# Performance work log

Measured on AMD Instinct MI355X. Metric: run time of the kernel, lower is better.

## Reference

```python
import jax, jax.numpy as jnp
import numpy as np

N_HEAD = 16
D_HEAD = 64
N_GROUPS = 4
D_EMBED = 1024
ROPE_N = 32
B, T = 2, 2048


def apply_rope(x, cos, sin):
    # x: (..., T, ROPE_N); cos/sin: (T, ROPE_N) broadcast over leading dims
    h = x.shape[-1]
    x1, x2 = x[..., : h // 2], x[..., h // 2 :]
    rotated = jnp.concatenate((-x2, x1), axis=-1)
    return (x * cos + rotated * sin).astype(x.dtype)


def setup_inputs() -> dict:
    key = jax.random.key(0)
    k1, k2, k3, k4, k5 = jax.random.split(key, 5)
    return {
        "x": jax.random.normal(k1, (B, T, D_EMBED), dtype=jnp.float32),
        "cos": jax.random.uniform(k2, (T, ROPE_N), dtype=jnp.float32),
        "sin": jax.random.uniform(k3, (T, ROPE_N), dtype=jnp.float32),
        "mask": jnp.ones((B, T), dtype=bool),  # unused by the original forward (passes None to SDPA)
        "Wqkv": jax.random.normal(k4, (D_EMBED, (N_HEAD + 2 * N_GROUPS) * D_HEAD), dtype=jnp.float32) * 0.02,
        "Wout": jax.random.normal(k5, (N_HEAD * D_HEAD, D_EMBED), dtype=jnp.float32) * 0.02,
    }


def reference(x, cos, sin, mask, Wqkv, Wout):
    Bv, Tv, _ = x.shape
    q_per_kv = N_HEAD // N_GROUPS  # 4
    total_qkv = q_per_kv + 2       # 6

    qkv = jnp.einsum("btc,cf->btf", x, Wqkv)  # (B, T, 1536)
    qkv = qkv.reshape(Bv, Tv, N_GROUPS, total_qkv, D_HEAD)
    qkv = jnp.transpose(qkv, (0, 2, 3, 1, 4))  # (B, G, total_qkv, T, d)

    q = qkv[:, :, :q_per_kv]           # (B, G, q_per_kv, T, d)
    k = qkv[:, :, q_per_kv : q_per_kv + 1]  # (B, G, 1, T, d)
    v = qkv[:, :, q_per_kv + 1 :]           # (B, G, 1, T, d)

    # GQA expand (1 < groups < heads)
    k = jnp.broadcast_to(k, (Bv, N_GROUPS, q_per_kv, Tv, D_HEAD))
    v = jnp.broadcast_to(v, (Bv, N_GROUPS, q_per_kv, Tv, D_HEAD))

    q = q.reshape(Bv, N_HEAD, Tv, D_HEAD)
    k = k.reshape(Bv, N_HEAD, Tv, D_HEAD)
    v = v.reshape(Bv, N_HEAD, Tv, D_HEAD)

    # partial RoPE on the first ROPE_N dims of each head
    q = jnp.concatenate((apply_rope(q[..., :ROPE_N], cos, sin), q[..., ROPE_N:]), axis=-1)
    k = jnp.concatenate((apply_rope(k[..., :ROPE_N], cos, sin), k[..., ROPE_N:]), axis=-1)

    scale = 1.0 / np.sqrt(D_HEAD).astype(np.float32)
    scores = jnp.einsum("bhtd,bhsd->bhts", q, k) * scale
    attn = jax.nn.softmax(scores, axis=-1)
    y = jnp.einsum("bhts,bhsd->bhtd", attn, v)   # (B, H, T, d)
    y = jnp.transpose(y, (0, 2, 1, 3)).reshape(Bv, Tv, N_HEAD * D_HEAD)
    return jnp.einsum("btf,fc->btc", y, Wout)
```

## Files before the change

### kernel.cpp

```cpp
#include <hip/hip_runtime.h>
#include <hip/hip_bf16.h>
#include <math.h>

#define BATCH   2
#define TSEQ    2048
#define DEMBED  1024
#define NHEAD   16
#define DHEAD   64
#define NGROUP  4
#define ROPEN   32
#define FQKV    1536
#define MROWS   (BATCH*TSEQ)

typedef __attribute__((ext_vector_type(8))) short short8;
typedef __attribute__((ext_vector_type(4))) float floatx4;

__device__ __forceinline__ void split_pack8(const float* f, uint4& h4, uint4& l4) {
    uint u[8], lu[8];
    #pragma unroll
    for (int j = 0; j < 8; ++j) {
        u[j] = __float_as_uint(f[j]);
        float lf = f[j] - __uint_as_float(u[j] & 0xffff0000u);
        lu[j] = __float_as_uint(lf);
    }
    h4.x = __builtin_amdgcn_perm(u[1], u[0], 0x07060302u);
    h4.y = __builtin_amdgcn_perm(u[3], u[2], 0x07060302u);
    h4.z = __builtin_amdgcn_perm(u[5], u[4], 0x07060302u);
    h4.w = __builtin_amdgcn_perm(u[7], u[6], 0x07060302u);
    l4.x = __builtin_amdgcn_perm(lu[1], lu[0], 0x07060302u);
    l4.y = __builtin_amdgcn_perm(lu[3], lu[2], 0x07060302u);
    l4.z = __builtin_amdgcn_perm(lu[5], lu[4], 0x07060302u);
    l4.w = __builtin_amdgcn_perm(lu[7], lu[6], 0x07060302u);
}

__device__ __forceinline__ void rtn_pack8(const float* f, uint4& h4) {
    uint t[8];
    #pragma unroll
    for (int j = 0; j < 8; ++j)
        t[j] = __float_as_uint(f[j]) + 0x8000u;
    h4.x = __builtin_amdgcn_perm(t[1], t[0], 0x07060302u);
    h4.y = __builtin_amdgcn_perm(t[3], t[2], 0x07060302u);
    h4.z = __builtin_amdgcn_perm(t[5], t[4], 0x07060302u);
    h4.w = __builtin_amdgcn_perm(t[7], t[6], 0x07060302u);
}

__device__ __forceinline__ ushort bf16_rtn(float x) {
    return (ushort)((__float_as_uint(x) + 0x8000u) >> 16);
}

__device__ __forceinline__ void lds_async16(void* lds, const void* gp) {
    __builtin_amdgcn_global_load_lds(
        (const __attribute__((address_space(1))) unsigned int*)gp,
        (__attribute__((address_space(3))) unsigned int*)lds,
        16, 0, 0);
}


__global__ __launch_bounds__(256) void conv_xy(const float* __restrict__ in,
                                               char* __restrict__ img) {
    const int tid = threadIdx.x;
    const int c   = blockIdx.x & 15;
    const int mt  = blockIdx.x >> 4;
    const int r    = tid >> 1;
    const int half = tid & 1;

    const float* src = in + (size_t)(mt*128 + r)*1024 + c*64 + half*32;
    float f[32];
    #pragma unroll
    for (int u = 0; u < 8; ++u)
        *(float4*)(f + 4*u) = *(const float4*)(src + 4*u);

    char* tile = img + ((size_t)(mt*16 + c)) * 32768;
    #pragma unroll
    for (int cc = 0; cc < 4; ++cc) {
        uint4 h4, l4;
        split_pack8(f + cc*8, h4, l4);
        int j    = half*4 + cc;
        int phys = j ^ (r & 7);
        *(uint4*)(tile + r*128 + phys*16)         = h4;
        *(uint4*)(tile + 16384 + r*128 + phys*16) = l4;
    }
}

__global__ __launch_bounds__(256) void conv_w(const float* __restrict__ W,
                                              int N,
                                              char* __restrict__ img) {
    __shared__ float Lf[64][132];
    const int tid = threadIdx.x;
    const int c   = blockIdx.x;
    const int nt  = blockIdx.y;

    {
        const int kk = tid >> 2;
        const int nc = (tid & 3) * 32;
        const float* src = W + (size_t)(c*64 + kk)*N + nt*128 + nc;
        #pragma unroll
        for (int u = 0; u < 8; ++u)
            *(float4*)(&Lf[kk][nc + 4*u]) = *(const float4*)(src + 4*u);
    }
    __syncthreads();

    char* tile = img + ((size_t)(nt*16 + c)) * 32768;
    #pragma unroll
    for (int rep = 0; rep < 4; ++rep) {
        int idx = rep*256 + tid;
        int n = idx & 127;
        int j = idx >> 7;
        float v[8];
        #pragma unroll
        for (int i = 0; i < 8; ++i) v[i] = Lf[j*8 + i][n];
        uint4 h4, l4;
        split_pack8(v, h4, l4);
        int phys = j ^ (n & 7);
        *(uint4*)(tile + n*128 + phys*16)         = h4;
        *(uint4*)(tile + 16384 + n*128 + phys*16) = l4;
    }
}

struct GemmAcc { floatx4 a[4][4]; };

__device__ __forceinline__ void gemm_mfma_core(const char* __restrict__ Aimg,
                                               const char* __restrict__ Bimg,
                                               char* smem, int mt, int nt,
                                               int tid, GemmAcc& G) {
    const int wv = tid >> 6;
    const int wm = wv & 1, wn = wv >> 1;
    const int lane = tid & 63;
    const int qd = lane >> 4, cl = lane & 15;
    const int wslot = (tid & 192) * 16;

    #pragma unroll
    for (int tm = 0; tm < 4; ++tm)
        #pragma unroll
        for (int tn = 0; tn < 4; ++tn)
            G.a[tm][tn] = (floatx4){0.f, 0.f, 0.f, 0.f};

    for (int c = 0; c < 16; ++c) {
        __syncthreads();
        {
            const uint4* gA = (const uint4*)(Aimg + ((size_t)(mt*16 + c)) * 32768) + tid;
            const uint4* gB = (const uint4*)(Bimg + ((size_t)(nt*16 + c)) * 32768) + tid;
            #pragma unroll
            for (int j = 0; j < 8; ++j) {
                lds_async16(smem + j*4096 + wslot,         gA + j*256);
                lds_async16(smem + 32768 + j*4096 + wslot, gB + j*256);
            }
        }
        __syncthreads();

        #pragma unroll
        for (int s = 0; s < 2; ++s) {
            const int phys = ((s*4 + qd) ^ (cl & 7)) * 16;
            short8 ah[4], al[4], bh[4], bl[4];
            #pragma unroll
            for (int tt = 0; tt < 4; ++tt) {
                const int rA = wm*64 + 16*tt + cl;
                ah[tt] = *(const short8*)(smem + rA*128 + phys);
                al[tt] = *(const short8*)(smem + 16384 + rA*128 + phys);
                const int rB = wn*64 + 16*tt + cl;
                bh[tt] = *(const short8*)(smem + 32768 + rB*128 + phys);
                bl[tt] = *(const short8*)(smem + 49152 + rB*128 + phys);
            }
            #pragma unroll
            for (int tm = 0; tm < 4; ++tm)
                #pragma unroll
                for (int tn = 0; tn < 4; ++tn) {
                    G.a[tm][tn] = __builtin_amdgcn_mfma_f32_16x16x32_bf16(ah[tm], bh[tn], G.a[tm][tn], 0, 0, 0);
                    G.a[tm][tn] = __builtin_amdgcn_mfma_f32_16x16x32_bf16(al[tm], bh[tn], G.a[tm][tn], 0, 0, 0);
                    G.a[tm][tn] = __builtin_amdgcn_mfma_f32_16x16x32_bf16(ah[tm], bl[tn], G.a[tm][tn], 0, 0, 0);
                }
        }
    }
}

__global__ __launch_bounds__(256, 2) void gemm_qkv_mfma(const char* __restrict__ Aimg,
                                                        const char* __restrict__ Bimg,
                                                        const float* __restrict__ cosp,
                                                        const float* __restrict__ sinp,
                                                        float* __restrict__ Qf,
                                                        ushort* __restrict__ Kimg,
                                                        ushort* __restrict__ Vimg) {
    __shared__ __align__(16) char smem[68608];
    const int tid = threadIdx.x;
    const int nt = blockIdx.x, mt = blockIdx.y;

    GemmAcc G;
    gemm_mfma_core(Aimg, Bimg, smem, mt, nt, tid, G);

    const int wv = tid >> 6;
    const int wm = wv & 1, wn = wv >> 1;
    const int lane = tid & 63;
    const int qd = lane >> 4, cl = lane & 15;

    const int slice = nt*2 + wn;
    const int g  = slice / 6;
    const int jj = slice % 6;
    const int b  = mt >> 4;

    if (jj != 5) {
        #pragma unroll
        for (int tm = 0; tm < 4; ++tm)
            #pragma unroll
            for (int r = 0; r < 4; ++r) {
                int m = mt*128 + wm*64 + 16*tm + 4*qd + r;
                int t = m & 2047;
                float c1 = cosp[t*ROPEN + cl],      s1 = sinp[t*ROPEN + cl];
                float c2 = cosp[t*ROPEN + 16 + cl], s2 = sinp[t*ROPEN + 16 + cl];
                float x1 = G.a[tm][0][r], x2 = G.a[tm][1][r];
                G.a[tm][0][r] = x1*c1 - x2*s1;
                G.a[tm][1][r] = x2*c2 + x1*s2;
            }
    }

    if (jj < 4) {
        #pragma unroll
        for (int tm = 0; tm < 4; ++tm)
            #pragma unroll
            for (int tn = 0; tn < 4; ++tn)
                #pragma unroll
                for (int r = 0; r < 4; ++r) {
                    int m = mt*128 + wm*64 + 16*tm + 4*qd + r;
                    Qf[(size_t)m*1024 + (g*4 + jj)*64 + 16*tn + cl] = G.a[tm][tn][r];
                }
    } else {
        float* Lw = (float*)(smem + wv*17152);
        __syncthreads();
        #pragma unroll
        for (int tm = 0; tm < 4; ++tm)
            #pragma unroll
            for (int tn = 0; tn < 4; ++tn)
                #pragma unroll
                for (int r = 0; r < 4; ++r)
                    Lw[(16*tm + 4*qd + r)*67 + 16*tn + cl] = G.a[tm][tn][r];
        __syncthreads();

        const int cloc = (mt & 15)*2 + wm;
        ushort* img = ((jj == 4) ? Kimg : Vimg)
                      + (size_t)(b*4 + g)*262144 + (size_t)cloc*8192;
        if (jj == 4) {
            const int rr = lane;
            float f[8];
            #pragma unroll
            for (int ch = 0; ch < 8; ++ch) {
                *(float4*)f       = *(const float4*)(&Lw[rr*67 + ch*8]);
                *(float4*)(f + 4) = *(const float4*)(&Lw[rr*67 + ch*8 + 4]);
                uint4 h4, l4;
                split_pack8(f, h4, l4);
                int phys = ch ^ (rr & 7);
                *(uint4*)(img + rr*64 + phys*8)        = h4;
                *(uint4*)(img + 4096 + rr*64 + phys*8) = l4;
            }
        } else {
            const int d = lane;
            float f[8];
            #pragma unroll
            for (int ch = 0; ch < 8; ++ch) {
                #pragma unroll
                for (int i = 0; i < 8; ++i) f[i] = Lw[(ch*8 + i)*67 + d];
                uint4 h4;
                rtn_pack8(f, h4);
                int phys = ch ^ (d & 7);
                *(uint4*)(img + d*64 + phys*8) = h4;
            }
        }
    }
}

__global__ __launch_bounds__(256, 2) void gemm_out_mfma(const char* __restrict__ Aimg,
                                                        const char* __restrict__ Bimg,
                                                        float* __restrict__ C) {
    __shared__ __align__(16) char smem[49152];
    const int tid = threadIdx.x;
    const int nt = blockIdx.x, mt = blockIdx.y;

    const int wv = tid >> 6;
    const int wm = wv & 1, wn = wv >> 1;
    const int lane = tid & 63;
    const int qd = lane >> 4, cl = lane & 15;
    const int wslot = (tid & 192) * 16;

    floatx4 acc[2][4];
    #pragma unroll
    for (int tm = 0; tm < 2; ++tm)
        #pragma unroll
        for (int tn = 0; tn < 4; ++tn)
            acc[tm][tn] = (floatx4){0.f, 0.f, 0.f, 0.f};

    for (int c = 0; c < 16; ++c) {
        __syncthreads();
        {
            const char* sA = Aimg + ((size_t)((mt >> 1)*16 + c))*32768
                                  + (mt & 1)*8192 + (size_t)tid*16;
            const char* sB = Bimg + ((size_t)(nt*16 + c))*32768 + (size_t)tid*16;
            lds_async16(smem + wslot,          sA);
            lds_async16(smem + 4096  + wslot,  sA + 4096);
            lds_async16(smem + 8192  + wslot,  sA + 16384);
            lds_async16(smem + 12288 + wslot,  sA + 16384 + 4096);
            #pragma unroll
            for (int j = 0; j < 4; ++j) {
                lds_async16(smem + 16384 + j*4096 + wslot, sB + j*4096);
                lds_async16(smem + 32768 + j*4096 + wslot, sB + 16384 + j*4096);
            }
        }
        __syncthreads();

        #pragma unroll
        for (int s = 0; s < 2; ++s) {
            const int phys = ((s*4 + qd) ^ (cl & 7)) * 16;
            short8 ah[2], al[2], bh[4], bl[4];
            #pragma unroll
            for (int tt = 0; tt < 2; ++tt) {
                const int rA = wm*32 + 16*tt + cl;
                ah[tt] = *(const short8*)(smem + rA*128 + phys);
                al[tt] = *(const short8*)(smem + 8192 + rA*128 + phys);
            }
            #pragma unroll
            for (int tt = 0; tt < 4; ++tt) {
                const int rB = wn*64 + 16*tt + cl;
                bh[tt] = *(const short8*)(smem + 16384 + rB*128 + phys);
                bl[tt] = *(const short8*)(smem + 32768 + rB*128 + phys);
            }
            #pragma unroll
            for (int tm = 0; tm < 2; ++tm)
                #pragma unroll
                for (int tn = 0; tn < 4; ++tn) {
                    acc[tm][tn] = __builtin_amdgcn_mfma_f32_16x16x32_bf16(ah[tm], bh[tn], acc[tm][tn], 0, 0, 0);
                    acc[tm][tn] = __builtin_amdgcn_mfma_f32_16x16x32_bf16(al[tm], bh[tn], acc[tm][tn], 0, 0, 0);
                    acc[tm][tn] = __builtin_amdgcn_mfma_f32_16x16x32_bf16(ah[tm], bl[tn], acc[tm][tn], 0, 0, 0);
                }
        }
    }

    #pragma unroll
    for (int tm = 0; tm < 2; ++tm)
        #pragma unroll
        for (int tn = 0; tn < 4; ++tn)
            #pragma unroll
            for (int r = 0; r < 4; ++r) {
                int m = mt*64 + wm*32 + 16*tm + 4*qd + r;
                int n = nt*128 + wn*64 + 16*tn + cl;
                C[(size_t)m*1024 + n] = acc[tm][tn][r];
            }
}

__global__ __launch_bounds__(256, 4) void attn8(const float* __restrict__ Qf,
                                                const char* __restrict__ Kimg,
                                                const char* __restrict__ Vimg,
                                                char* __restrict__ Yimg) {
    __shared__ __align__(16) char smem[20992];
    ushort* Pp = (ushort*)(smem + 16384);

    const int tid  = threadIdx.x;
    const int wv   = tid >> 6;
    const int lane = tid & 63;
    const int qd   = lane >> 4;
    const int cl   = lane & 15;

    const int bg    = blockIdx.x & 7;
    const int inner = blockIdx.x >> 3;
    const int hj    = inner >> 5;
    const int qt    = inner & 31;
    const int b = bg >> 2, g = bg & 3;
    const int h = g*4 + hj;

    short8 qh[2], ql[2];
    {
        const float* qp = Qf + (size_t)(b*2048 + qt*64 + wv*16 + cl)*1024
                             + h*64 + 8*qd;
        #pragma unroll
        for (int s = 0; s < 2; ++s) {
            float f[8];
            *(float4*)f       = *(const float4*)(qp + 32*s);
            *(float4*)(f + 4) = *(const float4*)(qp + 32*s + 4);
            #pragma unroll
            for (int i = 0; i < 8; ++i) f[i] *= 0.125f;
            uint4 h4, l4;
            split_pack8(f, h4, l4);
            qh[s] = __builtin_bit_cast(short8, h4);
            ql[s] = __builtin_bit_cast(short8, l4);
        }
    }

    floatx4 accO[4] = {};
    float lsum[4] = {};

    const char* Kg0 = Kimg + (size_t)bg*524288;
    const char* Vg0 = Vimg + (size_t)bg*524288;
    const int wslot = (tid & 192) * 16;

    {
        const char* src = Kg0 + (size_t)tid*16;
        lds_async16(smem + wslot,        src);
        lds_async16(smem + 4096 + wslot, src + 8192);
    }

    for (int c = 0; c < TSEQ/32; ++c) {
        __syncthreads();
        const int buf = c & 1;
        if (c + 1 < TSEQ/32) {
            const int nb = (c + 1) & 1;
            const char* src = Kg0 + (size_t)((c+1) >> 1)*16384
                                  + ((c+1) & 1)*4096 + (size_t)tid*16;
            lds_async16(smem + nb*8192 + wslot,        src);
            lds_async16(smem + nb*8192 + 4096 + wslot, src + 8192);
        }
        const char* Kl = smem + buf*8192;

        floatx4 accS[2] = {};
        __builtin_amdgcn_s_setprio(1);
        #pragma unroll
        for (int s = 0; s < 2; ++s) {
            #pragma unroll
            for (int tt = 0; tt < 2; ++tt) {
                const int off = (16*tt + cl)*128 + (((4*s + qd) ^ (cl & 7))*16);
                short8 bh = *(const short8*)(Kl + off);
                short8 bl = *(const short8*)(Kl + 4096 + off);
                accS[tt] = __builtin_amdgcn_mfma_f32_16x16x32_bf16(qh[s], bh, accS[tt], 0, 0, 0);
                accS[tt] = __builtin_amdgcn_mfma_f32_16x16x32_bf16(ql[s], bh, accS[tt], 0, 0, 0);
                accS[tt] = __builtin_amdgcn_mfma_f32_16x16x32_bf16(qh[s], bl, accS[tt], 0, 0, 0);
            }
        }
        __builtin_amdgcn_s_setprio(0);

        #pragma unroll
        for (int r = 0; r < 4; ++r) {
            float p0 = __expf(accS[0][r]);
            float p1 = __expf(accS[1][r]);
            lsum[r] += p0 + p1;
            ushort* prow = Pp + (16*wv + 4*qd + r)*36 + cl;
            prow[0]  = bf16_rtn(p0);
            prow[16] = bf16_rtn(p1);
        }

        const char* Vg = Vg0 + (size_t)(c >> 1)*16384;
        short8 pa = *(const short8*)(Pp + (16*wv + cl)*36 + 8*qd);
        __builtin_amdgcn_s_setprio(1);
        #pragma unroll
        for (int tt = 0; tt < 4; ++tt) {
            const int off = (16*tt + cl)*128 + ((((c & 1)*4 + qd) ^ (cl & 7))*16);
            short8 vh = *(const short8*)(Vg + off);
            accO[tt] = __builtin_amdgcn_mfma_f32_16x16x32_bf16(pa, vh, accO[tt], 0, 0, 0);
        }
        __builtin_amdgcn_s_setprio(0);
    }

    __syncthreads();
    float* Lt = (float*)smem;
    #pragma unroll
    for (int r = 0; r < 4; ++r) {
        float l = lsum[r];
        l += __shfl_xor(l, 1);
        l += __shfl_xor(l, 2);
        l += __shfl_xor(l, 4);
        l += __shfl_xor(l, 8);
        float inv = 1.0f / l;
        int row = 16*wv + 4*qd + r;
        Lt[row*66 + cl]      = accO[0][r] * inv;
        Lt[row*66 + 16 + cl] = accO[1][r] * inv;
        Lt[row*66 + 32 + cl] = accO[2][r] * inv;
        Lt[row*66 + 48 + cl] = accO[3][r] * inv;
    }
    __syncthreads();
    {
        const int r0 = tid >> 2;
        const int qq = tid & 3;
        float f[16];
        #pragma unroll
        for (int u = 0; u < 8; ++u)
            *(float2*)(f + 2*u) = *(const float2*)(&Lt[r0*66 + qq*16 + 2*u]);
        const int R = (qt & 1)*64 + r0;
        char* tile = Yimg + (size_t)((b*16 + (qt >> 1))*16 + h) * 32768;
        #pragma unroll
        for (int cc = 0; cc < 2; ++cc) {
            uint4 h4, l4;
            split_pack8(f + 8*cc, h4, l4);
            int j    = qq*2 + cc;
            int phys = j ^ (R & 7);
            *(uint4*)(tile + R*128 + phys*16)         = h4;
            *(uint4*)(tile + 16384 + R*128 + phys*16) = l4;
        }
    }
}

extern "C" void kernel_launch(void* const* d_in, const int* in_sizes, int n_in,
                              void* d_out, int out_size, void* d_ws, size_t ws_size,
                              hipStream_t stream) {
    const float* x    = (const float*)d_in[0];
    const float* cosp = (const float*)d_in[1];
    const float* sinp = (const float*)d_in[2];
    const float* Wqkv = (const float*)d_in[4];
    const float* Wout = (const float*)d_in[5];
    float* out = (float*)d_out;

    char* ws = (char*)d_ws;
    float*  Qf    = (float*)(ws);
    ushort* Kimg  = (ushort*)(ws + ((size_t)16<<20));
    ushort* Vimg  = (ushort*)(ws + ((size_t)20<<20));
    char*   Bo    = ws + ((size_t)24<<20);
    char*   Ximg  = ws + ((size_t)28<<20);
    char*   Bq    = ws + ((size_t)44<<20);
    char*   Yimg  = ws + ((size_t)28<<20);

    conv_xy<<<512, 256, 0, stream>>>(x, Ximg);
    conv_w<<<dim3(16, 12), 256, 0, stream>>>(Wqkv, FQKV, Bq);
    conv_w<<<dim3(16, 8), 256, 0, stream>>>(Wout, DEMBED, Bo);
    gemm_qkv_mfma<<<dim3(12, 32), 256, 0, stream>>>(Ximg, Bq, cosp, sinp,
                                                    Qf, Kimg, Vimg);
    attn8<<<1024, 256, 0, stream>>>(Qf, (const char*)Kimg, (const char*)Vimg,
                                    Yimg);
    gemm_out_mfma<<<dim3(8, 64), 256, 0, stream>>>(Yimg, Bo, out);
}
```

Baseline: 252.5 us.

## Shrink QKV GEMM tile to 64 rows, use exp2 softmax, precompute attention offsets

The QKV projection GEMM moves from 128x128 tiles to 64x128 tiles, reusing the gemm_out loader layout. This doubles the grid to 64 row-tiles and raises launch-bounds occupancy to 3, with the RoPE and K/V image epilogue rewritten for the smaller tile. The attention kernel folds log2(e) into the Q scale so it can call exp2f instead of __expf. It also precomputes the K, V and P LDS offsets outside the loop and unrolls the key loop by two. The trade-off is less operand reuse per GEMM block and higher register pressure in attention.

```diff
diff --git a/kernel.cpp b/kernel.cpp
--- a/kernel.cpp
+++ b/kernel.cpp
@@ -117,158 +117,13 @@
     }
 }
 
-struct GemmAcc { floatx4 a[4][4]; };
-
-__device__ __forceinline__ void gemm_mfma_core(const char* __restrict__ Aimg,
-                                               const char* __restrict__ Bimg,
-                                               char* smem, int mt, int nt,
-                                               int tid, GemmAcc& G) {
-    const int wv = tid >> 6;
-    const int wm = wv & 1, wn = wv >> 1;
-    const int lane = tid & 63;
-    const int qd = lane >> 4, cl = lane & 15;
-    const int wslot = (tid & 192) * 16;
-
-    #pragma unroll
-    for (int tm = 0; tm < 4; ++tm)
-        #pragma unroll
-        for (int tn = 0; tn < 4; ++tn)
-            G.a[tm][tn] = (floatx4){0.f, 0.f, 0.f, 0.f};
-
-    for (int c = 0; c < 16; ++c) {
-        __syncthreads();
-        {
-            const uint4* gA = (const uint4*)(Aimg + ((size_t)(mt*16 + c)) * 32768) + tid;
-            const uint4* gB = (const uint4*)(Bimg + ((size_t)(nt*16 + c)) * 32768) + tid;
-            #pragma unroll
-            for (int j = 0; j < 8; ++j) {
-                lds_async16(smem + j*4096 + wslot,         gA + j*256);
-                lds_async16(smem + 32768 + j*4096 + wslot, gB + j*256);
-            }
-        }
-        __syncthreads();
-
-        #pragma unroll
-        for (int s = 0; s < 2; ++s) {
-            const int phys = ((s*4 + qd) ^ (cl & 7)) * 16;
-            short8 ah[4], al[4], bh[4], bl[4];
-            #pragma unroll
-            for (int tt = 0; tt < 4; ++tt) {
-                const int rA = wm*64 + 16*tt + cl;
-                ah[tt] = *(const short8*)(smem + rA*128 + phys);
-                al[tt] = *(const short8*)(smem + 16384 + rA*128 + phys);
-                const int rB = wn*64 + 16*tt + cl;
-                bh[tt] = *(const short8*)(smem + 32768 + rB*128 + phys);
-                bl[tt] = *(const short8*)(smem + 49152 + rB*128 + phys);
-            }
-            #pragma unroll
-            for (int tm = 0; tm < 4; ++tm)
-                #pragma unroll
-                for (int tn = 0; tn < 4; ++tn) {
-                    G.a[tm][tn] = __builtin_amdgcn_mfma_f32_16x16x32_bf16(ah[tm], bh[tn], G.a[tm][tn], 0, 0, 0);
-                    G.a[tm][tn] = __builtin_amdgcn_mfma_f32_16x16x32_bf16(al[tm], bh[tn], G.a[tm][tn], 0, 0, 0);
-                    G.a[tm][tn] = __builtin_amdgcn_mfma_f32_16x16x32_bf16(ah[tm], bl[tn], G.a[tm][tn], 0, 0, 0);
-                }
-        }
-    }
-}
-
-__global__ __launch_bounds__(256, 2) void gemm_qkv_mfma(const char* __restrict__ Aimg,
+__global__ __launch_bounds__(256, 3) void gemm_qkv_mfma(const char* __restrict__ Aimg,
                                                         const char* __restrict__ Bimg,
                                                         const float* __restrict__ cosp,
                                                         const float* __restrict__ sinp,
                                                         float* __restrict__ Qf,
                                                         ushort* __restrict__ Kimg,
                                                         ushort* __restrict__ Vimg) {
-    __shared__ __align__(16) char smem[68608];
-    const int tid = threadIdx.x;
-    const int nt = blockIdx.x, mt = blockIdx.y;
-
-    GemmAcc G;
-    gemm_mfma_core(Aimg, Bimg, smem, mt, nt, tid, G);
-
-    const int wv = tid >> 6;
-    const int wm = wv & 1, wn = wv >> 1;
-    const int lane = tid & 63;
-    const int qd = lane >> 4, cl = lane & 15;
-
-    const int slice = nt*2 + wn;
-    const int g  = slice / 6;
-    const int jj = slice % 6;
-    const int b  = mt >> 4;
-
-    if (jj != 5) {
-        #pragma unroll
-        for (int tm = 0; tm < 4; ++tm)
-            #pragma unroll
-            for (int r = 0; r < 4; ++r) {
-                int m = mt*128 + wm*64 + 16*tm + 4*qd + r;
-                int t = m & 2047;
-                float c1 = cosp[t*ROPEN + cl],      s1 = sinp[t*ROPEN + cl];
-                float c2 = cosp[t*ROPEN + 16 + cl], s2 = sinp[t*ROPEN + 16 + cl];
-                float x1 = G.a[tm][0][r], x2 = G.a[tm][1][r];
-                G.a[tm][0][r] = x1*c1 - x2*s1;
-                G.a[tm][1][r] = x2*c2 + x1*s2;
-            }
-    }
-
-    if (jj < 4) {
-        #pragma unroll
-        for (int tm = 0; tm < 4; ++tm)
-            #pragma unroll
-            for (int tn = 0; tn < 4; ++tn)
-                #pragma unroll
-                for (int r = 0; r < 4; ++r) {
-                    int m = mt*128 + wm*64 + 16*tm + 4*qd + r;
-                    Qf[(size_t)m*1024 + (g*4 + jj)*64 + 16*tn + cl] = G.a[tm][tn][r];
-                }
-    } else {
-        float* Lw = (float*)(smem + wv*17152);
-        __syncthreads();
-        #pragma unroll
-        for (int tm = 0; tm < 4; ++tm)
-            #pragma unroll
-            for (int tn = 0; tn < 4; ++tn)
-                #pragma unroll
-                for (int r = 0; r < 4; ++r)
-                    Lw[(16*tm + 4*qd + r)*67 + 16*tn + cl] = G.a[tm][tn][r];
-        __syncthreads();
-
-        const int cloc = (mt & 15)*2 + wm;
-        ushort* img = ((jj == 4) ? Kimg : Vimg)
-                      + (size_t)(b*4 + g)*262144 + (size_t)cloc*8192;
-        if (jj == 4) {
-            const int rr = lane;
-            float f[8];
-            #pragma unroll
-            for (int ch = 0; ch < 8; ++ch) {
-                *(float4*)f       = *(const float4*)(&Lw[rr*67 + ch*8]);
-                *(float4*)(f + 4) = *(const float4*)(&Lw[rr*67 + ch*8 + 4]);
-                uint4 h4, l4;
-                split_pack8(f, h4, l4);
-                int phys = ch ^ (rr & 7);
-                *(uint4*)(img + rr*64 + phys*8)        = h4;
-                *(uint4*)(img + 4096 + rr*64 + phys*8) = l4;
-            }
-        } else {
-            const int d = lane;
-            float f[8];
-            #pragma unroll
-            for (int ch = 0; ch < 8; ++ch) {
-                #pragma unroll
-                for (int i = 0; i < 8; ++i) f[i] = Lw[(ch*8 + i)*67 + d];
-                uint4 h4;
-                rtn_pack8(f, h4);
-                int phys = ch ^ (d & 7);
-                *(uint4*)(img + d*64 + phys*8) = h4;
-            }
-        }
-    }
-}
-
-__global__ __launch_bounds__(256, 2) void gemm_out_mfma(const char* __restrict__ Aimg,
-                                                        const char* __restrict__ Bimg,
-                                                        float* __restrict__ C) {
     __shared__ __align__(16) char smem[49152];
     const int tid = threadIdx.x;
     const int nt = blockIdx.x, mt = blockIdx.y;
@@ -331,6 +186,148 @@
         }
     }
 
+    const int slice = nt*2 + wn;
+    const int g  = slice / 6;
+    const int jj = slice % 6;
+    const int b  = mt >> 5;
+
+    if (jj != 5) {
+        #pragma unroll
+        for (int tm = 0; tm < 2; ++tm)
+            #pragma unroll
+            for (int r = 0; r < 4; ++r) {
+                int m = mt*64 + wm*32 + 16*tm + 4*qd + r;
+                int t = m & 2047;
+                float c1 = cosp[t*ROPEN + cl],      s1 = sinp[t*ROPEN + cl];
+                float c2 = cosp[t*ROPEN + 16 + cl], s2 = sinp[t*ROPEN + 16 + cl];
+                float x1 = acc[tm][0][r], x2 = acc[tm][1][r];
+                acc[tm][0][r] = x1*c1 - x2*s1;
+                acc[tm][1][r] = x2*c2 + x1*s2;
+            }
+    }
+
+    if (jj < 4) {
+        #pragma unroll
+        for (int tm = 0; tm < 2; ++tm)
+            #pragma unroll
+            for (int tn = 0; tn < 4; ++tn)
+                #pragma unroll
+                for (int r = 0; r < 4; ++r) {
+                    int m = mt*64 + wm*32 + 16*tm + 4*qd + r;
+                    Qf[(size_t)m*1024 + (g*4 + jj)*64 + 16*tn + cl] = acc[tm][tn][r];
+                }
+    } else {
+        float* Lw = (float*)(smem + wn*17152);
+        __syncthreads();
+        #pragma unroll
+        for (int tm = 0; tm < 2; ++tm)
+            #pragma unroll
+            for (int tn = 0; tn < 4; ++tn)
+                #pragma unroll
+                for (int r = 0; r < 4; ++r)
+                    Lw[(wm*32 + 16*tm + 4*qd + r)*67 + 16*tn + cl] = acc[tm][tn][r];
+        __syncthreads();
+
+        const int cloc = mt & 31;
+        ushort* img = ((jj == 4) ? Kimg : Vimg)
+                      + (size_t)(b*4 + g)*262144 + (size_t)cloc*8192;
+        if (jj == 4) {
+            const int rr = wm*32 + (lane & 31);
+            const int cb = (lane >> 5) * 4;
+            float f[8];
+            #pragma unroll
+            for (int cc = 0; cc < 4; ++cc) {
+                const int ch = cb + cc;
+                *(float4*)f       = *(const float4*)(&Lw[rr*67 + ch*8]);
+                *(float4*)(f + 4) = *(const float4*)(&Lw[rr*67 + ch*8 + 4]);
+                uint4 h4, l4;
+                split_pack8(f, h4, l4);
+                int phys = ch ^ (rr & 7);
+                *(uint4*)(img + rr*64 + phys*8)        = h4;
+                *(uint4*)(img + 4096 + rr*64 + phys*8) = l4;
+            }
+        } else {
+            const int d = lane;
+            float f[8];
+            #pragma unroll
+            for (int cc = 0; cc < 4; ++cc) {
+                const int ch = wm*4 + cc;
+                #pragma unroll
+                for (int i = 0; i < 8; ++i) f[i] = Lw[(ch*8 + i)*67 + d];
+                uint4 h4;
+                rtn_pack8(f, h4);
+                int phys = ch ^ (d & 7);
+                *(uint4*)(img + d*64 + phys*8) = h4;
+            }
+        }
+    }
+}
+
+__global__ __launch_bounds__(256, 2) void gemm_out_mfma(const char* __restrict__ Aimg,
+                                                        const char* __restrict__ Bimg,
+                                                        float* __restrict__ C) {
+    __shared__ __align__(16) char smem[49152];
+    const int tid = threadIdx.x;
+    const int nt = blockIdx.x, mt = blockIdx.y;
+
+    const int wv = tid >> 6;
+    const int wm = wv & 1, wn = wv >> 1;
+    const int lane = tid & 63;
+    const int qd = lane >> 4, cl = lane & 15;
+    const int wslot = (tid & 192) * 16;
+
+    floatx4 acc[2][4];
+    #pragma unroll
+    for (int tm = 0; tm < 2; ++tm)
+        #pragma unroll
+        for (int tn = 0; tn < 4; ++tn)
+            acc[tm][tn] = (floatx4){0.f, 0.f, 0.f, 0.f};
+
+    for (int c = 0; c < 16; ++c) {
+        __syncthreads();
+        {
+            const char* sA = Aimg + ((size_t)((mt >> 1)*16 + c))*32768
+                                  + (mt & 1)*8192 + (size_t)tid*16;
+            const char* sB = Bimg + ((size_t)(nt*16 + c))*32768 + (size_t)tid*16;
+            lds_async16(smem + wslot,          sA);
+            lds_async16(smem + 4096  + wslot,  sA + 4096);
+            lds_async16(smem + 8192  + wslot,  sA + 16384);
+            lds_async16(smem + 12288 + wslot,  sA + 16384 + 4096);
+            #pragma unroll
+            for (int j = 0; j < 4; ++j) {
+                lds_async16(smem + 16384 + j*4096 + wslot, sB + j*4096);
+                lds_async16(smem + 32768 + j*4096 + wslot, sB + 16384 + j*4096);
+            }
+        }
+        __syncthreads();
+
+        #pragma unroll
+        for (int s = 0; s < 2; ++s) {
+            const int phys = ((s*4 + qd) ^ (cl & 7)) * 16;
+            short8 ah[2], al[2], bh[4], bl[4];
+            #pragma unroll
+            for (int tt = 0; tt < 2; ++tt) {
+                const int rA = wm*32 + 16*tt + cl;
+                ah[tt] = *(const short8*)(smem + rA*128 + phys);
+                al[tt] = *(const short8*)(smem + 8192 + rA*128 + phys);
+            }
+            #pragma unroll
+            for (int tt = 0; tt < 4; ++tt) {
+                const int rB = wn*64 + 16*tt + cl;
+                bh[tt] = *(const short8*)(smem + 16384 + rB*128 + phys);
+                bl[tt] = *(const short8*)(smem + 32768 + rB*128 + phys);
+            }
+            #pragma unroll
+            for (int tm = 0; tm < 2; ++tm)
+                #pragma unroll
+                for (int tn = 0; tn < 4; ++tn) {
+                    acc[tm][tn] = __builtin_amdgcn_mfma_f32_16x16x32_bf16(ah[tm], bh[tn], acc[tm][tn], 0, 0, 0);
+                    acc[tm][tn] = __builtin_amdgcn_mfma_f32_16x16x32_bf16(al[tm], bh[tn], acc[tm][tn], 0, 0, 0);
+                    acc[tm][tn] = __builtin_amdgcn_mfma_f32_16x16x32_bf16(ah[tm], bl[tn], acc[tm][tn], 0, 0, 0);
+                }
+        }
+    }
+
     #pragma unroll
     for (int tm = 0; tm < 2; ++tm)
         #pragma unroll
@@ -343,7 +340,7 @@
             }
 }
 
-__global__ __launch_bounds__(256, 4) void attn8(const float* __restrict__ Qf,
+__global__ __launch_bounds__(256, 4) void attn9(const float* __restrict__ Qf,
                                                 const char* __restrict__ Kimg,
                                                 const char* __restrict__ Vimg,
                                                 char* __restrict__ Yimg) {
@@ -373,7 +370,7 @@
             *(float4*)f       = *(const float4*)(qp + 32*s);
             *(float4*)(f + 4) = *(const float4*)(qp + 32*s + 4);
             #pragma unroll
-            for (int i = 0; i < 8; ++i) f[i] *= 0.125f;
+            for (int i = 0; i < 8; ++i) f[i] *= 0.125f * 1.44269504088896f;
             uint4 h4, l4;
             split_pack8(f, h4, l4);
             qh[s] = __builtin_bit_cast(short8, h4);
@@ -388,21 +385,34 @@
     const char* Vg0 = Vimg + (size_t)bg*524288;
     const int wslot = (tid & 192) * 16;
 
+    int kb[2];
+    #pragma unroll
+    for (int s = 0; s < 2; ++s)
+        kb[s] = cl*128 + (((4*s + qd) ^ (cl & 7)) * 16);
+    int voff[2][4];
+    #pragma unroll
+    for (int par = 0; par < 2; ++par)
+        #pragma unroll
+        for (int tt = 0; tt < 4; ++tt)
+            voff[par][tt] = (16*tt + cl)*128 + (((par*4 + qd) ^ (cl & 7)) * 16);
+    const int pst = (16*wv + 4*qd)*36 + cl;
+    const int pld = (16*wv + cl)*36 + 8*qd;
+
     {
         const char* src = Kg0 + (size_t)tid*16;
         lds_async16(smem + wslot,        src);
         lds_async16(smem + 4096 + wslot, src + 8192);
     }
 
+    #pragma unroll 2
     for (int c = 0; c < TSEQ/32; ++c) {
         __syncthreads();
         const int buf = c & 1;
         if (c + 1 < TSEQ/32) {
-            const int nb = (c + 1) & 1;
             const char* src = Kg0 + (size_t)((c+1) >> 1)*16384
                                   + ((c+1) & 1)*4096 + (size_t)tid*16;
-            lds_async16(smem + nb*8192 + wslot,        src);
-            lds_async16(smem + nb*8192 + 4096 + wslot, src + 8192);
+            lds_async16(smem + ((c+1) & 1)*8192 + wslot,        src);
+            lds_async16(smem + ((c+1) & 1)*8192 + 4096 + wslot, src + 8192);
         }
         const char* Kl = smem + buf*8192;
 
@@ -412,9 +422,8 @@
         for (int s = 0; s < 2; ++s) {
             #pragma unroll
             for (int tt = 0; tt < 2; ++tt) {
-                const int off = (16*tt + cl)*128 + (((4*s + qd) ^ (cl & 7))*16);
-                short8 bh = *(const short8*)(Kl + off);
-                short8 bl = *(const short8*)(Kl + 4096 + off);
+                short8 bh = *(const short8*)(Kl + kb[s] + tt*2048);
+                short8 bl = *(const short8*)(Kl + kb[s] + tt*2048 + 4096);
                 accS[tt] = __builtin_amdgcn_mfma_f32_16x16x32_bf16(qh[s], bh, accS[tt], 0, 0, 0);
                 accS[tt] = __builtin_amdgcn_mfma_f32_16x16x32_bf16(ql[s], bh, accS[tt], 0, 0, 0);
                 accS[tt] = __builtin_amdgcn_mfma_f32_16x16x32_bf16(qh[s], bl, accS[tt], 0, 0, 0);
@@ -424,21 +433,19 @@
 
         #pragma unroll
         for (int r = 0; r < 4; ++r) {
-            float p0 = __expf(accS[0][r]);
-            float p1 = __expf(accS[1][r]);
+            float p0 = exp2f(accS[0][r]);
+            float p1 = exp2f(accS[1][r]);
             lsum[r] += p0 + p1;
-            ushort* prow = Pp + (16*wv + 4*qd + r)*36 + cl;
-            prow[0]  = bf16_rtn(p0);
-            prow[16] = bf16_rtn(p1);
+            Pp[pst + r*36]      = bf16_rtn(p0);
+            Pp[pst + r*36 + 16] = bf16_rtn(p1);
         }
 
         const char* Vg = Vg0 + (size_t)(c >> 1)*16384;
-        short8 pa = *(const short8*)(Pp + (16*wv + cl)*36 + 8*qd);
+        short8 pa = *(const short8*)(Pp + pld);
         __builtin_amdgcn_s_setprio(1);
         #pragma unroll
         for (int tt = 0; tt < 4; ++tt) {
-            const int off = (16*tt + cl)*128 + ((((c & 1)*4 + qd) ^ (cl & 7))*16);
-            short8 vh = *(const short8*)(Vg + off);
+            short8 vh = *(const short8*)(Vg + voff[buf][tt]);
             accO[tt] = __builtin_amdgcn_mfma_f32_16x16x32_bf16(pa, vh, accO[tt], 0, 0, 0);
         }
         __builtin_amdgcn_s_setprio(0);
@@ -504,9 +511,9 @@
     conv_xy<<<512, 256, 0, stream>>>(x, Ximg);
     conv_w<<<dim3(16, 12), 256, 0, stream>>>(Wqkv, FQKV, Bq);
     conv_w<<<dim3(16, 8), 256, 0, stream>>>(Wout, DEMBED, Bo);
-    gemm_qkv_mfma<<<dim3(12, 32), 256, 0, stream>>>(Ximg, Bq, cosp, sinp,
+    gemm_qkv_mfma<<<dim3(12, 64), 256, 0, stream>>>(Ximg, Bq, cosp, sinp,
                                                     Qf, Kimg, Vimg);
-    attn8<<<1024, 256, 0, stream>>>(Qf, (const char*)Kimg, (const char*)Vimg,
+    attn9<<<1024, 256, 0, stream>>>(Qf, (const char*)Kimg, (const char*)Vimg,
                                     Yimg);
     gemm_out_mfma<<<dim3(8, 64), 256, 0, stream>>>(Yimg, Bo, out);
 }
```

Result: slower. 271.0 us (+7.3%).
